# Kernel tuning notes

Hardware: AMD Instinct MI355X
Metric: run time of the kernel (lower is better)

## Reference

```python
import jax, jax.numpy as jnp
import numpy as np

B, S, D, H, HD = 1, 4096, 1024, 16, 64
HALF = HD // 2


def setup_inputs() -> dict:
    key = jax.random.key(0)
    ks = jax.random.split(key, 8)
    std = 0.02
    x = jax.random.normal(ks[0], (B, S, D), dtype=jnp.float32)
    wq_w = jax.random.normal(ks[1], (D, D), dtype=jnp.float32) * std
    wk_w = jax.random.normal(ks[2], (D, D), dtype=jnp.float32) * std
    wv_w = jax.random.normal(ks[3], (D, D), dtype=jnp.float32) * std
    wo_w = jax.random.normal(ks[4], (D, D), dtype=jnp.float32) * std
    wq_b = jnp.zeros((D,), jnp.float32)
    wk_b = jnp.zeros((D,), jnp.float32)
    wv_b = jnp.zeros((D,), jnp.float32)
    wo_b = jnp.zeros((D,), jnp.float32)
    # LLaMA-style rotary frequencies: theta = 10000^{-2i/HD}
    inv_freq = 1.0 / (10000.0 ** (jnp.arange(0, HD, 2, dtype=jnp.float32) / HD))  # [HALF]
    t = jnp.arange(S, dtype=jnp.float32)
    angles = jnp.outer(t, inv_freq)  # [S, HALF]
    freqs_cos = jnp.cos(angles)
    freqs_sin = jnp.sin(angles)
    # causal additive mask (finite large-negative to stay grad-safe)
    mask = jnp.triu(jnp.full((S, S), -1e9, dtype=jnp.float32), k=1)[None, None]
    return {
        "x": x, "start_pos": 0, "freqs_cos": freqs_cos, "freqs_sin": freqs_sin,
        "mask": mask,
        "wq_w": wq_w, "wq_b": wq_b, "wk_w": wk_w, "wk_b": wk_b,
        "wv_w": wv_w, "wv_b": wv_b, "wo_w": wo_w, "wo_b": wo_b,
    }


def _apply_rope(t, cos, sin):
    # t: [B, S, H, HD]; cos/sin: [S, HALF]. Complex multiply on consecutive pairs.
    b, s, h, hd = t.shape
    t2 = t.reshape(b, s, h, hd // 2, 2)
    x0, x1 = t2[..., 0], t2[..., 1]
    c = cos[None, :, None, :]
    sn = sin[None, :, None, :]
    o0 = x0 * c - x1 * sn
    o1 = x0 * sn + x1 * c
    return jnp.stack([o0, o1], axis=-1).reshape(b, s, h, hd)


def reference(x, start_pos, freqs_cos, freqs_sin, mask,
              wq_w, wq_b, wk_w, wk_b, wv_w, wv_b, wo_w, wo_b):
    bsz, seqlen, dim = x.shape
    q = (x @ wq_w.T + wq_b).reshape(bsz, seqlen, H, HD)
    k = (x @ wk_w.T + wk_b).reshape(bsz, seqlen, H, HD)
    v = (x @ wv_w.T + wv_b).reshape(bsz, seqlen, H, HD)
    q = _apply_rope(q, freqs_cos, freqs_sin)
    k = _apply_rope(k, freqs_cos, freqs_sin)
    # [B, H, S, HD]
    q = q.transpose(0, 2, 1, 3)
    k = k.transpose(0, 2, 1, 3)
    v = v.transpose(0, 2, 1, 3)
    scores = jnp.einsum('bhqd,bhkd->bhqk', q, k) / jnp.sqrt(jnp.float32(HD))
    scores = scores + mask
    probs = jax.nn.softmax(scores.astype(jnp.float32), axis=-1).astype(q.dtype)
    out = jnp.einsum('bhqk,bhkd->bhqd', probs, v)  # [B, H, S, HD]
    out = out.transpose(0, 2, 1, 3).reshape(bsz, seqlen, dim)
    return out @ wo_w.T + wo_b
```

## Files before the change

### kernel.cpp

```cpp
#include <hip/hip_runtime.h>


#define S_LEN 4096
#define DIM   1024
#define NH    16
#define HD    64

typedef __attribute__((ext_vector_type(8))) short bf16x8;
typedef __attribute__((ext_vector_type(4))) float f32x4;

__device__ __forceinline__ unsigned short f2b(float f) {
  union { float f; unsigned int u; } v; v.f = f;
  unsigned int r = (v.u + 0x7fffu + ((v.u >> 16) & 1u)) >> 16;
  return (unsigned short)r;
}
__device__ __forceinline__ float b2f(unsigned short h) {
  union { unsigned int u; float f; } v; v.u = ((unsigned int)h) << 16;
  return v.f;
}
__device__ __forceinline__ unsigned int pk2t(float a, float b) {
  union { float f; unsigned int u; } x, y; x.f = a; y.f = b;
  return (x.u >> 16) | (y.u & 0xffff0000u);
}
__device__ __forceinline__ void gload16(const void* g, void* l) {
  __builtin_amdgcn_global_load_lds(
      (const __attribute__((address_space(1))) unsigned int*)g,
      (__attribute__((address_space(3))) unsigned int*)l, 16, 0, 0);
}
__device__ __forceinline__ f32x4 fzero4() { f32x4 z = {0.f, 0.f, 0.f, 0.f}; return z; }

__device__ __forceinline__ bf16x8 lds_swz(const unsigned short* s, int row, int chunk) {
  int byte = row * 128 + ((chunk ^ (row & 7)) << 4);
  return *(const bf16x8*)((const char*)s + byte);
}

__global__ void cvt_all(const float* __restrict__ x, const float* __restrict__ wq,
                        const float* __restrict__ wk, const float* __restrict__ wv,
                        const float* __restrict__ wo, const float* __restrict__ qb,
                        const float* __restrict__ kb, const float* __restrict__ vbs,
                        const float* __restrict__ ob, unsigned short* __restrict__ xb,
                        unsigned short* __restrict__ wqkvb, unsigned short* __restrict__ wobb,
                        float* __restrict__ biasq, float* __restrict__ biaso) {
  int i = blockIdx.x * 256 + threadIdx.x;
  if (i < 2097152) {
    const float* src; unsigned short* dst; int off;
    if (i < 1048576)      { src = x;  dst = xb;              off = i; }
    else if (i < 1310720) { src = wq; dst = wqkvb;           off = i - 1048576; }
    else if (i < 1572864) { src = wk; dst = wqkvb + 1048576; off = i - 1310720; }
    else if (i < 1835008) { src = wv; dst = wqkvb + 2097152; off = i - 1572864; }
    else                  { src = wo; dst = wobb;            off = i - 1835008; }
    float4 v = ((const float4*)src)[off];
    unsigned int lo = (unsigned int)f2b(v.x) | ((unsigned int)f2b(v.y) << 16);
    unsigned int hi = (unsigned int)f2b(v.z) | ((unsigned int)f2b(v.w) << 16);
    ((uint2*)dst)[off] = make_uint2(lo, hi);
  } else if (i < 2097152 + 1024) {
    int j = i - 2097152;
    if (j < 256)      ((float4*)biasq)[j]              = ((const float4*)qb)[j];
    else if (j < 512) ((float4*)(biasq + 1024))[j-256] = ((const float4*)kb)[j-256];
    else if (j < 768) ((float4*)(biasq + 2048))[j-512] = ((const float4*)vbs)[j-512];
    else              ((float4*)biaso)[j-768]          = ((const float4*)ob)[j-768];
  }
}

__global__ __launch_bounds__(512, 2) void gemm_qkv(
    const unsigned short* __restrict__ A, const unsigned short* __restrict__ B,
    const float* __restrict__ bias, unsigned short* __restrict__ dq,
    unsigned short* __restrict__ dk, unsigned short* __restrict__ vtout,
    const float* __restrict__ fc, const float* __restrict__ fs, int K) {
  __shared__ alignas(16) unsigned short sA[2][256 * 64];
  __shared__ alignas(16) unsigned short sB[2][256 * 64];
  const int tid = threadIdx.x;
  const int lane = tid & 63, wave = tid >> 6;
  const int ln = lane & 15, quad = lane >> 4;
  const int bm = blockIdx.x * 256, bn = blockIdx.y * 256;
  const int wr = (wave >> 2) * 128, wc = (wave & 3) * 64;

  f32x4 acc[8][4];
#pragma unroll
  for (int i = 0; i < 8; ++i)
#pragma unroll
    for (int j = 0; j < 4; ++j) acc[i][j] = fzero4();

#pragma unroll
  for (int i = 0; i < 4; ++i) {
    int o = (i * 512 + tid) * 8;
    int row = o >> 6, c = (o >> 3) & 7;
    int col = ((c ^ (row & 7)) << 3);
    gload16(A + (size_t)(bm + row) * K + col, (char*)sA[0] + o * 2);
    gload16(B + (size_t)(bn + row) * K + col, (char*)sB[0] + o * 2);
  }

  int buf = 0;
  for (int k0 = 0; k0 < K; k0 += 64, buf ^= 1) {
    __syncthreads();
    if (k0 + 64 < K) {
#pragma unroll
      for (int i = 0; i < 4; ++i) {
        int o = (i * 512 + tid) * 8;
        int row = o >> 6, c = (o >> 3) & 7;
        int col = k0 + 64 + ((c ^ (row & 7)) << 3);
        gload16(A + (size_t)(bm + row) * K + col, (char*)sA[buf ^ 1] + o * 2);
        gload16(B + (size_t)(bn + row) * K + col, (char*)sB[buf ^ 1] + o * 2);
      }
    }
#pragma unroll
    for (int ks = 0; ks < 2; ++ks) {
      bf16x8 af[8], bfr[4];
#pragma unroll
      for (int i = 0; i < 8; ++i)
        af[i] = lds_swz(sA[buf], wr + i * 16 + ln, ks * 4 + quad);
#pragma unroll
      for (int j = 0; j < 4; ++j)
        bfr[j] = lds_swz(sB[buf], wc + j * 16 + ln, ks * 4 + quad);
#pragma unroll
      for (int i = 0; i < 8; ++i)
#pragma unroll
        for (int j = 0; j < 4; ++j)
          acc[i][j] = __builtin_amdgcn_mfma_f32_16x16x32_bf16(af[i], bfr[j], acc[i][j], 0, 0, 0);
    }
  }

  const int bufi = bn >> 10;
  const int hq = ((bn & 1023) + wc) >> 6;
  if (bufi < 2) {
    unsigned short* const base = bufi == 0 ? dq : dk;
    const float qsc = bufi == 0 ? 0.180336880f : 1.0f;
#pragma unroll
    for (int i = 0; i < 8; ++i)
#pragma unroll
      for (int j = 0; j < 4; ++j) {
        int n = bn + wc + j * 16 + ln;
        float bi = bias[n];
        int hd = j * 16 + ln;
        int pi = hd >> 1;
        bool evn = (ln & 1) == 0;
#pragma unroll
        for (int r = 0; r < 4; ++r) {
          int m = bm + wr + i * 16 + quad * 4 + r;
          float val = acc[i][j][r] + bi;
          float par = __shfl_xor(val, 1);
          float c = fc[m * 32 + pi], sn = fs[m * 32 + pi];
          float o = evn ? (val * c - par * sn) : (par * sn + val * c);
          base[((size_t)(hq * S_LEN + m)) * HD + hd] = f2b(o * qsc);
        }
      }
  } else {
    __syncthreads();
    unsigned short* scr =
        (wave < 4 ? (unsigned short*)sA : (unsigned short*)sB) + (wave & 3) * 8192;
#pragma unroll
    for (int i = 0; i < 8; ++i)
#pragma unroll
      for (int j = 0; j < 4; ++j) {
        int n = bn + wc + j * 16 + ln;
        float bi = bias[n];
        int hd = j * 16 + ln;
#pragma unroll
        for (int r = 0; r < 4; ++r) {
          int sl = i * 16 + quad * 4 + r;
          int byte = hd * 256 + ((((sl >> 3) ^ (hd & 7)) << 4)) + (sl & 7) * 2;
          *(unsigned short*)((char*)scr + byte) = f2b(acc[i][j][r] + bi);
        }
      }
#pragma unroll
    for (int pass = 0; pass < 4; ++pass) {
      int row = pass * 16 + ln;
      uint4 d[4];
#pragma unroll
      for (int j = 0; j < 4; ++j) {
        int c = quad * 4 + j;
        d[j] = *(uint4*)((char*)scr + row * 256 + ((c ^ (row & 7)) << 4));
      }
      uint4* dst = (uint4*)(vtout + ((size_t)(hq * HD + row)) * S_LEN + bm + wr + quad * 32);
#pragma unroll
      for (int j = 0; j < 4; ++j) dst[j] = d[j];
    }
  }
}

__global__ __launch_bounds__(256) void gemm_out(
    const unsigned short* __restrict__ A, const unsigned short* __restrict__ B,
    const float* __restrict__ bias, float* __restrict__ outF, int N, int K) {
  __shared__ alignas(16) unsigned short sA[2][128 * 32];
  __shared__ alignas(16) unsigned short sB[2][64 * 32];
  const int tid = threadIdx.x;
  const int lane = tid & 63, wave = tid >> 6;
  const int ln = lane & 15, quad = lane >> 4;
  const int bm = blockIdx.x * 128, bn = blockIdx.y * 64;
  const int wr = (wave >> 1) * 64, wc = (wave & 1) * 32;

  f32x4 acc[4][2];
#pragma unroll
  for (int i = 0; i < 4; ++i)
#pragma unroll
    for (int j = 0; j < 2; ++j) acc[i][j] = fzero4();

  {
#pragma unroll
    for (int i = 0; i < 2; ++i) {
      int o = (i * 256 + tid) * 16;
      int e = o >> 1;
      int row = e >> 5, col = e & 31;
      gload16(A + (size_t)(bm + row) * K + col, (char*)sA[0] + o);
    }
    int o = tid * 16;
    int e = o >> 1;
    int row = e >> 5, col = e & 31;
    gload16(B + (size_t)(bn + row) * K + col, (char*)sB[0] + o);
  }

  int buf = 0;
  for (int k0 = 0; k0 < K; k0 += 32, buf ^= 1) {
    __syncthreads();
    if (k0 + 32 < K) {
#pragma unroll
      for (int i = 0; i < 2; ++i) {
        int o = (i * 256 + tid) * 16;
        int e = o >> 1;
        int row = e >> 5, col = e & 31;
        gload16(A + (size_t)(bm + row) * K + k0 + 32 + col, (char*)sA[buf ^ 1] + o);
      }
      int o = tid * 16;
      int e = o >> 1;
      int row = e >> 5, col = e & 31;
      gload16(B + (size_t)(bn + row) * K + k0 + 32 + col, (char*)sB[buf ^ 1] + o);
    }
    bf16x8 af[4], bfr[2];
#pragma unroll
    for (int i = 0; i < 4; ++i)
      af[i] = *(const bf16x8*)&sA[buf][(wr + i * 16 + ln) * 32 + quad * 8];
#pragma unroll
    for (int j = 0; j < 2; ++j)
      bfr[j] = *(const bf16x8*)&sB[buf][(wc + j * 16 + ln) * 32 + quad * 8];
#pragma unroll
    for (int i = 0; i < 4; ++i)
#pragma unroll
      for (int j = 0; j < 2; ++j)
        acc[i][j] = __builtin_amdgcn_mfma_f32_16x16x32_bf16(af[i], bfr[j], acc[i][j], 0, 0, 0);
  }

#pragma unroll
  for (int i = 0; i < 4; ++i)
#pragma unroll
    for (int j = 0; j < 2; ++j) {
      int n = bn + wc + j * 16 + ln;
      float bi = bias[n];
#pragma unroll
      for (int r = 0; r < 4; ++r) {
        int m = bm + wr + i * 16 + quad * 4 + r;
        outF[(size_t)m * N + n] = acc[i][j][r] + bi;
      }
    }
}

__global__ __launch_bounds__(512, 4) void flash_kernel(
    const unsigned short* __restrict__ qg, const unsigned short* __restrict__ kg,
    const unsigned short* __restrict__ vtg, unsigned short* __restrict__ attn) {
  __shared__ alignas(16) unsigned short sK[2][2][64 * 64];
  __shared__ alignas(16) unsigned short sV[2][2][64 * 64];

  const int tid = threadIdx.x;
  const int lane = tid & 63, wave = tid >> 6;
  const int w = wave & 3, grp = wave >> 2;
  const int ln = lane & 15, quad = lane >> 4;
  const int c = blockIdx.x;
  const int h = c & 15;
  const int qt = 63 - (c >> 4);
  const int qrow = qt * 64 + w * 16;

  const unsigned short* qh = qg + (size_t)h * (S_LEN * HD);
  const unsigned short* kh = kg + (size_t)h * (S_LEN * HD);
  const unsigned short* vh = vtg + (size_t)h * (HD * S_LEN);

  bf16x8 qf[2];
  qf[0] = *(const bf16x8*)(qh + (size_t)(qrow + ln) * HD + quad * 8);
  qf[1] = *(const bf16x8*)(qh + (size_t)(qrow + ln) * HD + 32 + quad * 8);

  f32x4 o_acc[4];
  f32x4 l_acc = fzero4();
#pragma unroll
  for (int t = 0; t < 4; ++t) o_acc[t] = fzero4();
  bf16x8 ones;
#pragma unroll
  for (int j = 0; j < 8; ++j) ones[j] = (short)0x3F80;

  const int nst = (qt + 2) >> 1;
  const int srow = tid >> 3, sch = tid & 7;
  const int kswz = (sch ^ (srow & 7)) << 3;

  gload16(kh + (size_t)srow * HD + kswz, (char*)sK[0][0] + tid * 16);
  gload16(kh + (size_t)(64 + srow) * HD + kswz, (char*)sK[0][1] + tid * 16);
  gload16(vh + (size_t)srow * S_LEN + kswz, (char*)sV[0][0] + tid * 16);
  gload16(vh + (size_t)srow * S_LEN + 64 + kswz, (char*)sV[0][1] + tid * 16);

  int buf = 0;
  for (int s = 0; s < nst; ++s, buf ^= 1) {
    __syncthreads();
    if (s + 1 < nst) {
      const int kvE = (2 * s + 2) * 64, kvO = kvE + 64;
      gload16(kh + (size_t)(kvE + srow) * HD + kswz, (char*)sK[buf ^ 1][0] + tid * 16);
      gload16(kh + (size_t)(kvO + srow) * HD + kswz, (char*)sK[buf ^ 1][1] + tid * 16);
      gload16(vh + (size_t)srow * S_LEN + kvE + kswz, (char*)sV[buf ^ 1][0] + tid * 16);
      gload16(vh + (size_t)srow * S_LEN + kvO + kswz, (char*)sV[buf ^ 1][1] + tid * 16);
    }
    const int kt = 2 * s + grp;
    if (kt > qt) continue;
    const unsigned short* kp = sK[buf][grp];
    const unsigned short* vp = sV[buf][grp];

    f32x4 sc[4];
#pragma unroll
    for (int t = 0; t < 4; ++t) sc[t] = fzero4();
#pragma unroll
    for (int t = 0; t < 4; ++t) {
      bf16x8 kb0 = lds_swz(kp, t * 16 + ln, quad);
      bf16x8 kb1 = lds_swz(kp, t * 16 + ln, 4 + quad);
      sc[t] = __builtin_amdgcn_mfma_f32_16x16x32_bf16(kb0, qf[0], sc[t], 0, 0, 0);
      sc[t] = __builtin_amdgcn_mfma_f32_16x16x32_bf16(kb1, qf[1], sc[t], 0, 0, 0);
    }

    float e[4][4];
    if (kt == qt) {
#pragma unroll
      for (int t = 0; t < 4; ++t)
#pragma unroll
        for (int r = 0; r < 4; ++r) {
          int kvl = 16 * t + quad * 4 + r;
          e[t][r] = (kvl <= w * 16 + ln) ? __builtin_amdgcn_exp2f(sc[t][r]) : 0.0f;
        }
    } else {
#pragma unroll
      for (int t = 0; t < 4; ++t)
#pragma unroll
        for (int r = 0; r < 4; ++r) e[t][r] = __builtin_amdgcn_exp2f(sc[t][r]);
    }

    unsigned int x0 = pk2t(e[0][0], e[0][1]), x1 = pk2t(e[0][2], e[0][3]);
    unsigned int y0 = pk2t(e[1][0], e[1][1]), y1 = pk2t(e[1][2], e[1][3]);
    unsigned int z0 = pk2t(e[2][0], e[2][1]), z1 = pk2t(e[2][2], e[2][3]);
    unsigned int w0 = pk2t(e[3][0], e[3][1]), w1 = pk2t(e[3][2], e[3][3]);
    auto a32 = __builtin_amdgcn_permlane32_swap(x0, y0, false, false);
    auto a16 = __builtin_amdgcn_permlane16_swap(a32[0], a32[1], false, false);
    auto b32 = __builtin_amdgcn_permlane32_swap(x1, y1, false, false);
    auto b16 = __builtin_amdgcn_permlane16_swap(b32[0], b32[1], false, false);
    auto c32 = __builtin_amdgcn_permlane32_swap(z0, w0, false, false);
    auto c16 = __builtin_amdgcn_permlane16_swap(c32[0], c32[1], false, false);
    auto d32 = __builtin_amdgcn_permlane32_swap(z1, w1, false, false);
    auto d16 = __builtin_amdgcn_permlane16_swap(d32[0], d32[1], false, false);
    union { uint4 u; bf16x8 b; } pa0u, pa1u;
    pa0u.u = make_uint4(a16[0], b16[0], a16[1], b16[1]);
    pa1u.u = make_uint4(c16[0], d16[0], c16[1], d16[1]);
    const bf16x8 pa0 = pa0u.b, pa1 = pa1u.b;

    l_acc = __builtin_amdgcn_mfma_f32_16x16x32_bf16(pa0, ones, l_acc, 0, 0, 0);
    l_acc = __builtin_amdgcn_mfma_f32_16x16x32_bf16(pa1, ones, l_acc, 0, 0, 0);

#pragma unroll
    for (int t = 0; t < 4; ++t) {
      bf16x8 vb0 = lds_swz(vp, t * 16 + ln, quad);
      bf16x8 vb1 = lds_swz(vp, t * 16 + ln, 4 + quad);
      o_acc[t] = __builtin_amdgcn_mfma_f32_16x16x32_bf16(pa0, vb0, o_acc[t], 0, 0, 0);
      o_acc[t] = __builtin_amdgcn_mfma_f32_16x16x32_bf16(pa1, vb1, o_acc[t], 0, 0, 0);
    }
  }

  __syncthreads();
  float* mrg = (float*)sK;
  const int mi = (w * 64 + lane) * 20;
  if (grp == 1) {
    *(f32x4*)&mrg[mi +  0] = o_acc[0];
    *(f32x4*)&mrg[mi +  4] = o_acc[1];
    *(f32x4*)&mrg[mi +  8] = o_acc[2];
    *(f32x4*)&mrg[mi + 12] = o_acc[3];
    *(f32x4*)&mrg[mi + 16] = l_acc;
  }
  __syncthreads();
  if (grp == 0) {
    o_acc[0] += *(const f32x4*)&mrg[mi + 0];
    o_acc[1] += *(const f32x4*)&mrg[mi + 4];
    o_acc[2] += *(const f32x4*)&mrg[mi + 8];
    o_acc[3] += *(const f32x4*)&mrg[mi + 12];
    l_acc += *(const f32x4*)&mrg[mi + 16];
    float inv[4];
#pragma unroll
    for (int r = 0; r < 4; ++r) inv[r] = 1.0f / l_acc[r];
#pragma unroll
    for (int t = 0; t < 4; ++t)
#pragma unroll
      for (int r = 0; r < 4; ++r) {
        int row = qrow + quad * 4 + r;
        attn[(size_t)row * DIM + h * HD + t * 16 + ln] = f2b(o_acc[t][r] * inv[r]);
      }
  }
}

extern "C" void kernel_launch(void* const* d_in, const int* in_sizes, int n_in,
                              void* d_out, int out_size, void* d_ws, size_t ws_size,
                              hipStream_t stream) {
  const float* x    = (const float*)d_in[0];
  const float* fc   = (const float*)d_in[2];
  const float* fs   = (const float*)d_in[3];
  const float* wqw  = (const float*)d_in[5];
  const float* wqb  = (const float*)d_in[6];
  const float* wkw  = (const float*)d_in[7];
  const float* wkb  = (const float*)d_in[8];
  const float* wvw  = (const float*)d_in[9];
  const float* wvb  = (const float*)d_in[10];
  const float* wow  = (const float*)d_in[11];
  const float* wobf = (const float*)d_in[12];
  float* out = (float*)d_out;

  char* ws = (char*)d_ws;
  const size_t MB = (size_t)1 << 20;
  unsigned short* xb    = (unsigned short*)(ws + 0);
  unsigned short* wqkvb = (unsigned short*)(ws + 8 * MB);
  unsigned short* wobb  = (unsigned short*)(ws + 16 * MB);
  float* biasq = (float*)(ws + 18 * MB);
  float* biaso = (float*)(ws + 18 * MB + 65536);
  unsigned short* qb_ = (unsigned short*)(ws + 19 * MB);
  unsigned short* kb_ = (unsigned short*)(ws + 27 * MB);
  unsigned short* vt  = (unsigned short*)(ws + 35 * MB);
  unsigned short* attn = (unsigned short*)(ws + 0);

  cvt_all<<<8196, 256, 0, stream>>>(x, wqw, wkw, wvw, wow, wqb, wkb, wvb, wobf,
                                    xb, wqkvb, wobb, biasq, biaso);
  gemm_qkv<<<dim3(16, 12), 512, 0, stream>>>(xb, wqkvb, biasq, qb_, kb_, vt, fc, fs, 1024);
  flash_kernel<<<1024, 512, 0, stream>>>(qb_, kb_, vt, attn);
  gemm_out<<<dim3(32, 16), 256, 0, stream>>>(attn, wobb, biaso, out, 1024, 1024);
}
```

Measured before the change: 248.9 us.

## Interleave QKV GEMM global loads with MFMA phases using fine-grained barriers

Restructures the QKV projection GEMM main loop into four phases per K-tile. Each phase loads a subset of A/B fragments from LDS, issues one chunk of the next tile's global-to-LDS copy, and runs a 4x4 block of MFMAs under raised wave priority, with explicit s_waitcnt vmcnt/lgkmcnt and s_barrier calls in place of __syncthreads. The goal is to spread global loads across compute and overlap LDS reads with MFMA issue. The loop count is hardcoded to 16 tiles, which assumes K=1024. A missing barrier before the V-transpose scratch readback is also added.

```diff
diff --git a/kernel.cpp b/kernel.cpp
--- a/kernel.cpp
+++ b/kernel.cpp
@@ -74,6 +74,7 @@
   const int ln = lane & 15, quad = lane >> 4;
   const int bm = blockIdx.x * 256, bn = blockIdx.y * 256;
   const int wr = (wave >> 2) * 128, wc = (wave & 3) * 64;
+  const int NT = K >> 6;
 
   f32x4 acc[8][4];
 #pragma unroll
@@ -81,44 +82,92 @@
 #pragma unroll
     for (int j = 0; j < 4; ++j) acc[i][j] = fzero4();
 
-#pragma unroll
-  for (int i = 0; i < 4; ++i) {
-    int o = (i * 512 + tid) * 8;
-    int row = o >> 6, c = (o >> 3) & 7;
-    int col = ((c ^ (row & 7)) << 3);
-    gload16(A + (size_t)(bm + row) * K + col, (char*)sA[0] + o * 2);
-    gload16(B + (size_t)(bn + row) * K + col, (char*)sB[0] + o * 2);
-  }
-
-  int buf = 0;
-  for (int k0 = 0; k0 < K; k0 += 64, buf ^= 1) {
-    __syncthreads();
-    if (k0 + 64 < K) {
-#pragma unroll
-      for (int i = 0; i < 4; ++i) {
-        int o = (i * 512 + tid) * 8;
-        int row = o >> 6, c = (o >> 3) & 7;
-        int col = k0 + 64 + ((c ^ (row & 7)) << 3);
-        gload16(A + (size_t)(bm + row) * K + col, (char*)sA[buf ^ 1] + o * 2);
-        gload16(B + (size_t)(bn + row) * K + col, (char*)sB[buf ^ 1] + o * 2);
-      }
-    }
-#pragma unroll
-    for (int ks = 0; ks < 2; ++ks) {
-      bf16x8 af[8], bfr[4];
-#pragma unroll
-      for (int i = 0; i < 8; ++i)
-        af[i] = lds_swz(sA[buf], wr + i * 16 + ln, ks * 4 + quad);
+#define STAGE(tt, ch) do {                                                   \
+    int o_ = ((ch) * 512 + tid) * 8;                                         \
+    int row_ = o_ >> 6, c_ = (o_ >> 3) & 7;                                  \
+    int col_ = ((tt) << 6) + ((c_ ^ (row_ & 7)) << 3);                       \
+    int bs_ = (tt) & 1;                                                      \
+    gload16(A + (size_t)(bm + row_) * K + col_, (char*)sA[bs_] + o_ * 2);    \
+    gload16(B + (size_t)(bn + row_) * K + col_, (char*)sB[bs_] + o_ * 2);    \
+  } while (0)
+#define BAR()   __builtin_amdgcn_s_barrier()
+#define LGKM0() asm volatile("s_waitcnt lgkmcnt(0)" ::: "memory")
+
+  STAGE(0, 0); STAGE(0, 1); STAGE(0, 2); STAGE(0, 3); STAGE(1, 0);
+  asm volatile("s_waitcnt vmcnt(2)" ::: "memory");
+  BAR();
+
+#pragma unroll 2
+  for (int t = 0; t < 16; ++t) {
+    const unsigned short* cA = sA[t & 1];
+    const unsigned short* cB = sB[t & 1];
+    bf16x8 a0[4], a1[4], b0[4], b1[4];
+
+#pragma unroll
+    for (int j = 0; j < 4; ++j) b0[j] = lds_swz(cB, wc + j * 16 + ln, quad);
+#pragma unroll
+    for (int i = 0; i < 4; ++i) a0[i] = lds_swz(cA, wr + i * 16 + ln, quad);
+    if (t + 1 < NT) STAGE(t + 1, 1);
+    BAR(); LGKM0();
+    __builtin_amdgcn_s_setprio(1);
+#pragma unroll
+    for (int i = 0; i < 4; ++i)
 #pragma unroll
       for (int j = 0; j < 4; ++j)
-        bfr[j] = lds_swz(sB[buf], wc + j * 16 + ln, ks * 4 + quad);
-#pragma unroll
-      for (int i = 0; i < 8; ++i)
-#pragma unroll
-        for (int j = 0; j < 4; ++j)
-          acc[i][j] = __builtin_amdgcn_mfma_f32_16x16x32_bf16(af[i], bfr[j], acc[i][j], 0, 0, 0);
-    }
-  }
+        acc[i][j] = __builtin_amdgcn_mfma_f32_16x16x32_bf16(a0[i], b0[j], acc[i][j], 0, 0, 0);
+    __builtin_amdgcn_s_setprio(0);
+    BAR();
+
+#pragma unroll
+    for (int i = 0; i < 4; ++i) a1[i] = lds_swz(cA, wr + (i + 4) * 16 + ln, quad);
+#pragma unroll
+    for (int j = 0; j < 4; ++j) b1[j] = lds_swz(cB, wc + j * 16 + ln, 4 + quad);
+    if (t + 1 < NT) STAGE(t + 1, 2);
+    BAR(); LGKM0();
+    __builtin_amdgcn_s_setprio(1);
+#pragma unroll
+    for (int i = 0; i < 4; ++i)
+#pragma unroll
+      for (int j = 0; j < 4; ++j)
+        acc[i + 4][j] = __builtin_amdgcn_mfma_f32_16x16x32_bf16(a1[i], b0[j], acc[i + 4][j], 0, 0, 0);
+    __builtin_amdgcn_s_setprio(0);
+    BAR();
+
+#pragma unroll
+    for (int i = 0; i < 4; ++i) a0[i] = lds_swz(cA, wr + i * 16 + ln, 4 + quad);
+#pragma unroll
+    for (int i = 0; i < 4; ++i) a1[i] = lds_swz(cA, wr + (i + 4) * 16 + ln, 4 + quad);
+    if (t + 1 < NT) STAGE(t + 1, 3);
+    BAR(); LGKM0();
+    __builtin_amdgcn_s_setprio(1);
+#pragma unroll
+    for (int i = 0; i < 4; ++i)
+#pragma unroll
+      for (int j = 0; j < 4; ++j)
+        acc[i][j] = __builtin_amdgcn_mfma_f32_16x16x32_bf16(a0[i], b1[j], acc[i][j], 0, 0, 0);
+    __builtin_amdgcn_s_setprio(0);
+    BAR();
+
+    if (t + 2 < NT) STAGE(t + 2, 0);
+    BAR(); LGKM0();
+    __builtin_amdgcn_s_setprio(1);
+#pragma unroll
+    for (int i = 0; i < 4; ++i)
+#pragma unroll
+      for (int j = 0; j < 4; ++j)
+        acc[i + 4][j] = __builtin_amdgcn_mfma_f32_16x16x32_bf16(a1[i], b1[j], acc[i + 4][j], 0, 0, 0);
+    __builtin_amdgcn_s_setprio(0);
+    if (t < 14) {
+      asm volatile("s_waitcnt vmcnt(2)" ::: "memory");
+      BAR();
+    } else if (t == 14) {
+      asm volatile("s_waitcnt vmcnt(0)" ::: "memory");
+      BAR();
+    }
+  }
+#undef STAGE
+#undef BAR
+#undef LGKM0
 
   const int bufi = bn >> 10;
   const int hq = ((bn & 1023) + wc) >> 6;
@@ -162,6 +211,7 @@
           *(unsigned short*)((char*)scr + byte) = f2b(acc[i][j][r] + bi);
         }
       }
+    __syncthreads();
 #pragma unroll
     for (int pass = 0; pass < 4; ++pass) {
       int row = pass * 16 + ln;
```

New measurement: 248.2 us. No clear change (-0.3%).
